# Kernel optimization log

Measured on AMD Instinct MI355X. Metric: run time of the kernel, lower is better.

The kernel has to match this reference:

```python
import jax, jax.numpy as jnp
import numpy as np
import math

V, D, H, L, T, B = 50257, 1024, 16, 8, 1024, 4
HD = D // H
EPS = 1e-5


def setup_inputs() -> dict:
    key = jax.random.key(0)
    ks = jax.random.split(key, 8)
    s = 0.02
    inp = {
        'context': jax.random.randint(ks[0], (B, T), 0, V, dtype=jnp.int32),
        'targets': jax.random.randint(ks[1], (B, T), 0, V, dtype=jnp.int32),
        'wte': jax.random.normal(ks[2], (V, D), jnp.float32) * s,  # tied with lm_head
        'wpe': jax.random.normal(ks[3], (T, D), jnp.float32) * s,
        'ln1_g': jnp.ones((L, D), jnp.float32), 'ln1_b': jnp.zeros((L, D), jnp.float32),
        'w_attn': jax.random.normal(ks[4], (L, 3 * D, D), jnp.float32) * s,
        'w_proj': jax.random.normal(ks[5], (L, D, D), jnp.float32) * s,
        'ln2_g': jnp.ones((L, D), jnp.float32), 'ln2_b': jnp.zeros((L, D), jnp.float32),
        'w_fc': jax.random.normal(ks[6], (L, 4 * D, D), jnp.float32) * s,
        'w_out': jax.random.normal(ks[7], (L, D, 4 * D), jnp.float32) * s,
        'lnf_g': jnp.ones((D,), jnp.float32), 'lnf_b': jnp.zeros((D,), jnp.float32),
    }
    return inp


def layer_norm(x, g, b):
    mu = jnp.mean(x, axis=-1, keepdims=True)
    var = jnp.var(x, axis=-1, keepdims=True)
    return (x - mu) * jax.lax.rsqrt(var + EPS) * g + b


def attention(x, w_attn, w_proj):
    # x: [B,T,D]; w_attn: [3D,D] (torch Linear convention: y = x @ W^T)
    qkv = x @ w_attn.T  # [B,T,3D]
    q, k, v = jnp.split(qkv, 3, axis=-1)
    q = q.reshape(B, T, H, HD).transpose(0, 2, 1, 3)  # [B,H,T,hd]
    k = k.reshape(B, T, H, HD).transpose(0, 2, 1, 3)
    v = v.reshape(B, T, H, HD).transpose(0, 2, 1, 3)
    att = jnp.einsum('bhtd,bhsd->bhts', q, k) * (1.0 / math.sqrt(HD))
    causal = jnp.tril(jnp.ones((T, T), dtype=bool))
    att = jnp.where(causal, att, -jnp.inf)
    att = jax.nn.softmax(att, axis=-1)
    y = jnp.einsum('bhts,bhsd->bhtd', att, v)
    y = y.transpose(0, 2, 1, 3).reshape(B, T, D)
    return y @ w_proj.T


def mlp(x, w_fc, w_out):
    h = jax.nn.gelu(x @ w_fc.T, approximate=False)  # exact GELU = torch nn.GELU()
    return h @ w_out.T


def reference(context, targets, wte, wpe, ln1_g, ln1_b, w_attn, w_proj,
              ln2_g, ln2_b, w_fc, w_out, lnf_g, lnf_b):
    x = wte[context] + wpe[jnp.arange(T)]  # [B,T,D]
    for i in range(L):
        x = x + attention(layer_norm(x, ln1_g[i], ln1_b[i]), w_attn[i], w_proj[i])
        x = x + mlp(layer_norm(x, ln2_g[i], ln2_b[i]), w_fc[i], w_out[i])
    x = layer_norm(x, lnf_g, lnf_b)
    logits = x @ wte.T  # tied lm_head, [B,T,V]
    # cross entropy with ignore_index=-1
    logp = jax.nn.log_softmax(logits, axis=-1)
    tgt = targets.reshape(-1)
    valid = tgt != -1
    safe_tgt = jnp.where(valid, tgt, 0)
    nll = -jnp.take_along_axis(logp.reshape(-1, V), safe_tgt[:, None], axis=-1)[:, 0]
    loss = jnp.sum(jnp.where(valid, nll, 0.0)) / jnp.maximum(jnp.sum(valid), 1)
    return logits, loss
```

## Files before the change

### kernel.cpp

```cpp
#include <hip/hip_runtime.h>
#include <cstdint>

#define V_SIZE 50257
#define V_PAD  50432
#define D_DIM  1024
#define H_NUM  16
#define L_NUM  8
#define T_LEN  1024
#define B_NUM  4
#define HD_DIM 64
#define M_ROWS 4096
#define LN_EPS 1e-5f

typedef __attribute__((ext_vector_type(8))) __bf16 bf16x8;
typedef __attribute__((ext_vector_type(4))) float f32x4;
typedef __attribute__((ext_vector_type(8))) unsigned short u16x8;

__device__ __forceinline__ unsigned short f2bf(float f) {
  unsigned u = __builtin_bit_cast(unsigned, f);
  u += 0x7fffu + ((u >> 16) & 1u);
  return (unsigned short)(u >> 16);
}

__device__ __forceinline__ void gload_lds16(const void* g, void* l) {
  typedef const __attribute__((address_space(1))) unsigned int* gp_t;
  typedef __attribute__((address_space(3))) unsigned int* lp_t;
  __builtin_amdgcn_global_load_lds((gp_t)g, (lp_t)l, 16, 0, 0);
}

__device__ __forceinline__ f32x4 mfma16(bf16x8 a, bf16x8 b, f32x4 c) {
  return __builtin_amdgcn_mfma_f32_16x16x32_bf16(a, b, c, 0, 0, 0);
}

#define BARSB() { __builtin_amdgcn_s_barrier(); __builtin_amdgcn_sched_barrier(0); }
#define SCHB()  __builtin_amdgcn_sched_barrier(0)

__global__ __launch_bounds__(256) void embed_kernel(const int* __restrict__ ctx,
                                                    const float* __restrict__ wte,
                                                    const float* __restrict__ wpe,
                                                    float* __restrict__ x) {
  int i = blockIdx.x * blockDim.x + threadIdx.x;
  if (i >= M_ROWS * D_DIM) return;
  int bt = i / D_DIM, d = i - bt * D_DIM;
  int t = bt & (T_LEN - 1);
  x[i] = wte[(size_t)ctx[bt] * D_DIM + d] + wpe[(size_t)t * D_DIM + d];
}

__global__ __launch_bounds__(256) void conv_layer_kernel(const float* __restrict__ wa,
                                                         const float* __restrict__ wp,
                                                         const float* __restrict__ wf,
                                                         const float* __restrict__ wo,
                                                         unsigned short* __restrict__ oa,
                                                         unsigned short* __restrict__ op,
                                                         unsigned short* __restrict__ of,
                                                         unsigned short* __restrict__ oo) {
  long i = (long)(blockIdx.x * 256 + threadIdx.x) * 8;
  const float* src; unsigned short* dst; long off;
  if (i < 3145728L)      { src = wa; dst = oa; off = i; }
  else if (i < 4194304L) { src = wp; dst = op; off = i - 3145728L; }
  else if (i < 8388608L) { src = wf; dst = of; off = i - 4194304L; }
  else                   { src = wo; dst = oo; off = i - 8388608L; }
  float4 v0 = *(const float4*)(src + off);
  float4 v1 = *(const float4*)(src + off + 4);
  u16x8 o;
  o[0] = f2bf(v0.x); o[1] = f2bf(v0.y); o[2] = f2bf(v0.z); o[3] = f2bf(v0.w);
  o[4] = f2bf(v1.x); o[5] = f2bf(v1.y); o[6] = f2bf(v1.z); o[7] = f2bf(v1.w);
  *(u16x8*)(dst + off) = o;
}

__global__ __launch_bounds__(256) void conv_kernel(const float* __restrict__ in,
                                                   unsigned short* __restrict__ out, long n) {
  long i = (long)(blockIdx.x * 256 + threadIdx.x) * 8;
  if (i >= n) return;
  float4 v0 = *(const float4*)(in + i);
  float4 v1 = *(const float4*)(in + i + 4);
  u16x8 o;
  o[0] = f2bf(v0.x); o[1] = f2bf(v0.y); o[2] = f2bf(v0.z); o[3] = f2bf(v0.w);
  o[4] = f2bf(v1.x); o[5] = f2bf(v1.y); o[6] = f2bf(v1.z); o[7] = f2bf(v1.w);
  *(u16x8*)(out + i) = o;
}

__global__ __launch_bounds__(256) void layernorm_kernel(const float* __restrict__ x,
                                                        const float* __restrict__ g,
                                                        const float* __restrict__ b,
                                                        unsigned short* __restrict__ o) {
  int r = blockIdx.x;
  int tid = threadIdx.x;
  const float* row = x + (size_t)r * D_DIM;
  float4 v = *(const float4*)(row + tid * 4);
  float s  = v.x + v.y + v.z + v.w;
  float s2 = v.x * v.x + v.y * v.y + v.z * v.z + v.w * v.w;
  #pragma unroll
  for (int off = 32; off; off >>= 1) {
    s  += __shfl_xor(s, off);
    s2 += __shfl_xor(s2, off);
  }
  __shared__ float a1[4], a2[4];
  int w = tid >> 6, lane = tid & 63;
  if (lane == 0) { a1[w] = s; a2[w] = s2; }
  __syncthreads();
  s  = a1[0] + a1[1] + a1[2] + a1[3];
  s2 = a2[0] + a2[1] + a2[2] + a2[3];
  float mu  = s * (1.0f / D_DIM);
  float var = s2 * (1.0f / D_DIM) - mu * mu;
  float rs  = rsqrtf(var + LN_EPS);
  int d = tid * 4;
  float4 gv = *(const float4*)(g + d);
  float4 bv = *(const float4*)(b + d);
  ushort4 ov;
  ov.x = f2bf((v.x - mu) * rs * gv.x + bv.x);
  ov.y = f2bf((v.y - mu) * rs * gv.y + bv.y);
  ov.z = f2bf((v.z - mu) * rs * gv.z + bv.z);
  ov.w = f2bf((v.w - mu) * rs * gv.w + bv.w);
  *(ushort4*)(o + (size_t)r * D_DIM + d) = ov;
}

template<int EPI>
__global__ __launch_bounds__(256) void mfma_gemm(const unsigned short* __restrict__ A,
                                                 const unsigned short* __restrict__ W,
                                                 const float* R, void* Cout,
                                                 int K, int ldc, int nreal) {
  __shared__ unsigned short As[128 * 32];
  __shared__ unsigned short Bs[128 * 32];
  const int tid  = threadIdx.x;
  const int wave = tid >> 6, lane = tid & 63;
  const int wr = wave >> 1, wc = wave & 1;
  const long row0 = (long)blockIdx.y * 128;
  const long col0 = (long)blockIdx.x * 128;
  f32x4 acc[4][4] = {};
  const int frow = lane & 15;
  const int fk   = (lane >> 4) * 8;
  const int b0 = wave * 2048 + lane * 16;
  for (int k0 = 0; k0 < K; k0 += 32) {
    #pragma unroll
    for (int c = 0; c < 2; ++c) {
      int b = b0 + c * 1024;
      int r = b >> 6, ke = (b & 63) >> 1;
      gload_lds16(A + (row0 + r) * (long)K + k0 + ke, (char*)As + b);
      gload_lds16(W + (col0 + r) * (long)K + k0 + ke, (char*)Bs + b);
    }
    __syncthreads();
    bf16x8 af[4], bfr[4];
    #pragma unroll
    for (int i = 0; i < 4; ++i)
      af[i] = *(const bf16x8*)(As + (wr * 64 + i * 16 + frow) * 32 + fk);
    #pragma unroll
    for (int j = 0; j < 4; ++j)
      bfr[j] = *(const bf16x8*)(Bs + (wc * 64 + j * 16 + frow) * 32 + fk);
    #pragma unroll
    for (int i = 0; i < 4; ++i)
      #pragma unroll
      for (int j = 0; j < 4; ++j)
        acc[i][j] = mfma16(af[i], bfr[j], acc[i][j]);
    __syncthreads();
  }
  const int crow = (lane >> 4) * 4;
  const int ccol = lane & 15;
  #pragma unroll
  for (int i = 0; i < 4; ++i) {
    #pragma unroll
    for (int r = 0; r < 4; ++r) {
      long row = row0 + wr * 64 + i * 16 + crow + r;
      #pragma unroll
      for (int j = 0; j < 4; ++j) {
        long col = col0 + wc * 64 + j * 16 + ccol;
        float v = acc[i][j][r];
        if (EPI == 1) {
          ((float*)Cout)[row * (long)ldc + col] = v + R[row * (long)ldc + col];
        } else {
          ((float*)Cout)[row * (long)ldc + col] = v;
        }
      }
    }
  }
}

__device__ __forceinline__ void stage_chunk8(const unsigned short* __restrict__ base,
                                             long rbase, int K, long gk,
                                             char* cb, int tid) {
  #pragma unroll
  for (int j = 0; j < 2; ++j) {
    int db = j * 8192 + tid * 16;
    int lb = db ^ (((db >> 7) & 3) << 4);
    long r = lb >> 6;
    int e = (lb & 63) >> 1;
    gload_lds16(base + (rbase + r) * (long)K + gk + e, cb + db);
  }
}

__device__ __forceinline__ bf16x8 rdfrag(const char* cb, int rr, int lhi) {
  int p = (rr << 6) + (lhi << 4);
  p ^= ((rr >> 1) & 3) << 4;
  return *(const bf16x8*)(cb + p);
}

template<int EPI>
__global__ __launch_bounds__(512, 1) void gemm8p(const unsigned short* __restrict__ A,
                                                 const unsigned short* __restrict__ W,
                                                 void* Cout, int K, int ldc, int nreal,
                                                 int nbx, int xcd) {
  __shared__ char lds[131072];
  const int tid  = threadIdx.x;
  const int lane = tid & 63;
  const int wave = tid >> 6;
  const int wr = wave >> 2, wc = wave & 3;
  const int lhi = lane >> 4, llo = lane & 15;
  int bid = blockIdx.x;
  if (xcd) { int per = (int)gridDim.x >> 3; bid = (bid & 7) * per + (bid >> 3); }
  const int brow = bid % nbx;
  const int bcol = bid / nbx;
  const long row0 = (long)brow * 256;
  const long col0 = (long)bcol * 256;
  char* Ab0 = (char*)lds;
  char* Bb0 = (char*)lds + 65536;
  const int nt = K >> 6;

  stage_chunk8(W, col0, K, 0,  Bb0,         tid);
  stage_chunk8(A, row0, K, 0,  Ab0,         tid);
  stage_chunk8(W, col0, K, 32, Bb0 + 16384, tid);
  stage_chunk8(A, row0, K, 32, Ab0 + 16384, tid);
  stage_chunk8(W, col0, K, 64, Bb0 + 32768, tid);
  stage_chunk8(A, row0, K, 64, Ab0 + 32768, tid);
  stage_chunk8(W, col0, K, 96, Bb0 + 49152, tid);
  asm volatile("s_waitcnt vmcnt(10)" ::: "memory");
  BARSB();

  const int arow  = wr * 128 + llo;
  const int brow_ = wc * 64 + llo;

  bf16x8 aa0[4], aa1[4], bb0[4], bb1[4];
  #pragma unroll
  for (int m = 0; m < 4; ++m) aa0[m] = rdfrag(Ab0, arow + m * 16, lhi);
  #pragma unroll
  for (int n = 0; n < 4; ++n) bb0[n] = rdfrag(Bb0, brow_ + n * 16, lhi);

  f32x4 acc[8][4] = {};
  for (int t = 0; t < nt; ++t) {
    char* Ac = Ab0 + (t & 1) * 32768;
    char* Bc = Bb0 + (t & 1) * 32768;
    char* An = Ab0 + ((t + 1) & 1) * 32768;
    char* Bn = Bb0 + ((t + 1) & 1) * 32768;
    #pragma unroll
    for (int m = 0; m < 4; ++m) aa1[m] = rdfrag(Ac, arow + 64 + m * 16, lhi);
    asm volatile("s_waitcnt lgkmcnt(4)" ::: "memory");
    SCHB();
    if (t + 1 < nt) stage_chunk8(A, row0, K, (long)(t + 1) * 64 + 32, An + 16384, tid);
    __builtin_amdgcn_s_setprio(1);
    #pragma unroll
    for (int m = 0; m < 4; ++m)
      #pragma unroll
      for (int n = 0; n < 4; ++n)
        acc[m][n] = mfma16(aa0[m], bb0[n], acc[m][n]);
    __builtin_amdgcn_s_setprio(0);
    SCHB();
    if (t < nt - 1) { asm volatile("s_waitcnt vmcnt(8)" ::: "memory"); }
    else            { asm volatile("s_waitcnt vmcnt(0)" ::: "memory"); }
    BARSB();
    #pragma unroll
    for (int m = 0; m < 4; ++m) aa0[m] = rdfrag(Ac + 16384, arow + m * 16, lhi);
    #pragma unroll
    for (int n = 0; n < 4; ++n) bb1[n] = rdfrag(Bc + 16384, brow_ + n * 16, lhi);
    asm volatile("s_waitcnt lgkmcnt(8)" ::: "memory");
    SCHB();
    if (t + 2 < nt) stage_chunk8(W, col0, K, (long)(t + 2) * 64, Bc, tid);
    __builtin_amdgcn_s_setprio(1);
    #pragma unroll
    for (int m = 0; m < 4; ++m)
      #pragma unroll
      for (int n = 0; n < 4; ++n)
        acc[m + 4][n] = mfma16(aa1[m], bb0[n], acc[m + 4][n]);
    __builtin_amdgcn_s_setprio(0);
    SCHB();
    BARSB();
    #pragma unroll
    for (int m = 0; m < 4; ++m) aa1[m] = rdfrag(Ac + 16384, arow + 64 + m * 16, lhi);
    asm volatile("s_waitcnt lgkmcnt(4)" ::: "memory");
    SCHB();
    if (t + 2 < nt) stage_chunk8(A, row0, K, (long)(t + 2) * 64, Ac, tid);
    __builtin_amdgcn_s_setprio(1);
    #pragma unroll
    for (int m = 0; m < 4; ++m)
      #pragma unroll
      for (int n = 0; n < 4; ++n)
        acc[m][n] = mfma16(aa0[m], bb1[n], acc[m][n]);
    __builtin_amdgcn_s_setprio(0);
    SCHB();
    if (t <= nt - 3)      { asm volatile("s_waitcnt vmcnt(8)" ::: "memory"); }
    else if (t == nt - 2) { asm volatile("s_waitcnt vmcnt(4)" ::: "memory"); }
    else                  { asm volatile("s_waitcnt vmcnt(0)" ::: "memory"); }
    BARSB();
    if (t + 1 < nt) {
      #pragma unroll
      for (int m = 0; m < 4; ++m) aa0[m] = rdfrag(An, arow + m * 16, lhi);
      #pragma unroll
      for (int n = 0; n < 4; ++n) bb0[n] = rdfrag(Bn, brow_ + n * 16, lhi);
      asm volatile("s_waitcnt lgkmcnt(8)" ::: "memory");
    } else {
      asm volatile("s_waitcnt lgkmcnt(0)" ::: "memory");
    }
    SCHB();
    if (t + 2 < nt) stage_chunk8(W, col0, K, (long)(t + 2) * 64 + 32, Bc + 16384, tid);
    __builtin_amdgcn_s_setprio(1);
    #pragma unroll
    for (int m = 0; m < 4; ++m)
      #pragma unroll
      for (int n = 0; n < 4; ++n)
        acc[m + 4][n] = mfma16(aa1[m], bb1[n], acc[m + 4][n]);
    __builtin_amdgcn_s_setprio(0);
    SCHB();
    BARSB();
  }

  #pragma unroll
  for (int mi = 0; mi < 8; ++mi) {
    #pragma unroll
    for (int rg = 0; rg < 4; ++rg) {
      long row = row0 + wr * 128 + mi * 16 + lhi * 4 + rg;
      #pragma unroll
      for (int n = 0; n < 4; ++n) {
        long col = col0 + wc * 64 + n * 16 + llo;
        float v = acc[mi][n][rg];
        if (EPI == 0) {
          if (col < nreal) ((float*)Cout)[row * (long)ldc + col] = v;
        } else if (EPI == 2) {
          float gl = 0.5f * v * (1.0f + erff(v * 0.70710678118654752440f));
          ((unsigned short*)Cout)[row * (long)ldc + col] = f2bf(gl);
        } else {
          ((unsigned short*)Cout)[row * (long)ldc + col] = f2bf(v);
        }
      }
    }
  }
}

__global__ __launch_bounds__(256) void flash_attn_kernel(const unsigned short* __restrict__ qkv,
                                                         unsigned short* __restrict__ y) {
  __shared__ unsigned short Kls[64 * 64];
  __shared__ unsigned short Vtls[64 * 64];
  __shared__ unsigned short Pls[4][16 * 64];
  const int tid = threadIdx.x, wave = tid >> 6, lane = tid & 63;
  const int qt = blockIdx.x;
  const int h = blockIdx.y & (H_NUM - 1), b = blockIdx.y >> 4;
  const int q0 = qt * 64;
  const int lhi = lane >> 4, llo = lane & 15;

  const int qrow = q0 + wave * 16 + llo;
  const unsigned short* qptr =
      qkv + ((size_t)(b * T_LEN + qrow)) * 3072 + h * HD_DIM + lhi * 8;
  const bf16x8 qa0 = *(const bf16x8*)qptr;
  const bf16x8 qa1 = *(const bf16x8*)(qptr + 32);

  f32x4 o[4] = {};
  float m[4] = {-1e30f, -1e30f, -1e30f, -1e30f};
  float l[4] = {0.f, 0.f, 0.f, 0.f};

  const unsigned short* kg = qkv + (size_t)b * T_LEN * 3072 + D_DIM + h * HD_DIM;
  const unsigned short* vg = kg + D_DIM;

  const int krow = tid >> 2, kcol = (tid & 3) * 16;
  const int vs0 = (tid >> 3) * 2, vd0 = (tid & 7) * 8;

  const int ntiles = qt + 1;
  for (int st = 0; st < ntiles; ++st) {
    const int s0 = st * 64;
    {
      const unsigned short* src = kg + (size_t)(s0 + krow) * 3072 + kcol;
      u16x8 a = *(const u16x8*)src;
      u16x8 c = *(const u16x8*)(src + 8);
      int base = krow * 128 + kcol * 2;
      int sw = (krow & 7) << 4;
      *(u16x8*)((char*)Kls + ((base) ^ sw))      = a;
      *(u16x8*)((char*)Kls + ((base + 16) ^ sw)) = c;
    }
    {
      const unsigned short* src = vg + (size_t)(s0 + vs0) * 3072 + vd0;
      u16x8 a = *(const u16x8*)src;
      u16x8 c = *(const u16x8*)(src + 3072);
      #pragma unroll
      for (int j = 0; j < 8; ++j) {
        int d = vd0 + j;
        unsigned val = (unsigned)a[j] | ((unsigned)c[j] << 16);
        *(unsigned*)((char*)Vtls + ((d * 128 + vs0 * 2) ^ ((d & 7) << 4))) = val;
      }
    }
    __syncthreads();

    f32x4 s_acc[4] = {};
    #pragma unroll
    for (int kt = 0; kt < 4; ++kt) {
      int kr = kt * 16 + llo;
      int sw = (kr & 7) << 4;
      bf16x8 kb0 = *(const bf16x8*)((char*)Kls + ((kr * 128 + lhi * 16) ^ sw));
      bf16x8 kb1 = *(const bf16x8*)((char*)Kls + ((kr * 128 + 64 + lhi * 16) ^ sw));
      s_acc[kt] = mfma16(qa0, kb0, s_acc[kt]);
      s_acc[kt] = mfma16(qa1, kb1, s_acc[kt]);
    }

    float p[4][4];
    float tmax[4] = {-1e30f, -1e30f, -1e30f, -1e30f};
    const int qg = q0 + wave * 16 + lhi * 4;
    #pragma unroll
    for (int kt = 0; kt < 4; ++kt) {
      int ks = s0 + kt * 16 + llo;
      #pragma unroll
      for (int r = 0; r < 4; ++r) {
        float sv = (ks <= qg + r) ? s_acc[kt][r] * 0.125f : -1e30f;
        p[kt][r] = sv;
        tmax[r] = fmaxf(tmax[r], sv);
      }
    }
    #pragma unroll
    for (int r = 0; r < 4; ++r) {
      #pragma unroll
      for (int off = 1; off < 16; off <<= 1)
        tmax[r] = fmaxf(tmax[r], __shfl_xor(tmax[r], off));
      float mn = fmaxf(m[r], tmax[r]);
      float corr = __expf(m[r] - mn);
      m[r] = mn;
      float ps = 0.f;
      #pragma unroll
      for (int kt = 0; kt < 4; ++kt) {
        p[kt][r] = __expf(p[kt][r] - mn);
        ps += p[kt][r];
      }
      #pragma unroll
      for (int off = 1; off < 16; off <<= 1)
        ps += __shfl_xor(ps, off);
      l[r] = l[r] * corr + ps;
      #pragma unroll
      for (int dt = 0; dt < 4; ++dt) o[dt][r] *= corr;
    }

    unsigned short* pw = Pls[wave];
    #pragma unroll
    for (int r = 0; r < 4; ++r) {
      int q = lhi * 4 + r;
      int sw = (q & 7) << 4;
      #pragma unroll
      for (int kt = 0; kt < 4; ++kt) {
        int k = kt * 16 + llo;
        *(unsigned short*)((char*)pw + ((q * 128 + k * 2) ^ sw)) = f2bf(p[kt][r]);
      }
    }
    asm volatile("s_waitcnt lgkmcnt(0)" ::: "memory");

    int psw = (llo & 7) << 4;
    bf16x8 pa0 = *(const bf16x8*)((char*)pw + ((llo * 128 + lhi * 16) ^ psw));
    bf16x8 pa1 = *(const bf16x8*)((char*)pw + ((llo * 128 + 64 + lhi * 16) ^ psw));
    #pragma unroll
    for (int dt = 0; dt < 4; ++dt) {
      int vr = dt * 16 + llo;
      int sw = (vr & 7) << 4;
      bf16x8 vb0 = *(const bf16x8*)((char*)Vtls + ((vr * 128 + lhi * 16) ^ sw));
      bf16x8 vb1 = *(const bf16x8*)((char*)Vtls + ((vr * 128 + 64 + lhi * 16) ^ sw));
      o[dt] = mfma16(pa0, vb0, o[dt]);
      o[dt] = mfma16(pa1, vb1, o[dt]);
    }
    __syncthreads();
  }

  #pragma unroll
  for (int r = 0; r < 4; ++r) {
    long row = q0 + wave * 16 + lhi * 4 + r;
    float inv = 1.0f / l[r];
    #pragma unroll
    for (int dt = 0; dt < 4; ++dt) {
      long col = h * HD_DIM + dt * 16 + llo;
      y[(row + (size_t)b * T_LEN) * D_DIM + col] = f2bf(o[dt][r] * inv);
    }
  }
}

__global__ __launch_bounds__(256) void loss_rows_kernel(const float* __restrict__ logits,
                                                        const int* __restrict__ tgt,
                                                        float* __restrict__ nll,
                                                        float* __restrict__ vld) {
  int r = blockIdx.x;
  int tid = threadIdx.x;
  const float* row = logits + (size_t)r * V_SIZE;
  float lm = -1e30f, ls = 0.f;
  for (int i = tid; i < V_SIZE; i += 256) {
    float v = row[i];
    float nm = fmaxf(lm, v);
    ls = ls * __expf(lm - nm) + __expf(v - nm);
    lm = nm;
  }
  #pragma unroll
  for (int off = 1; off < 64; off <<= 1) {
    float om = __shfl_xor(lm, off);
    float os = __shfl_xor(ls, off);
    float nm = fmaxf(lm, om);
    ls = ls * __expf(lm - nm) + os * __expf(om - nm);
    lm = nm;
  }
  __shared__ float sm[4], ss[4];
  int w = tid >> 6, lane = tid & 63;
  if (lane == 0) { sm[w] = lm; ss[w] = ls; }
  __syncthreads();
  if (tid == 0) {
    lm = sm[0]; ls = ss[0];
    #pragma unroll
    for (int i = 1; i < 4; ++i) {
      float nm = fmaxf(lm, sm[i]);
      ls = ls * __expf(lm - nm) + ss[i] * __expf(sm[i] - nm);
      lm = nm;
    }
    int tg = tgt[r];
    if (tg != -1) { nll[r] = lm + logf(ls) - row[tg]; vld[r] = 1.0f; }
    else          { nll[r] = 0.f;                     vld[r] = 0.f; }
  }
}

__global__ __launch_bounds__(256) void loss_reduce_kernel(const float* __restrict__ nll,
                                                          const float* __restrict__ vld,
                                                          float* __restrict__ out) {
  int tid = threadIdx.x;
  float s = 0.f, c = 0.f;
  for (int i = tid; i < M_ROWS; i += 256) { s += nll[i]; c += vld[i]; }
  #pragma unroll
  for (int off = 32; off; off >>= 1) { s += __shfl_xor(s, off); c += __shfl_xor(c, off); }
  __shared__ float s1[4], s2[4];
  int w = tid >> 6, lane = tid & 63;
  if (lane == 0) { s1[w] = s; s2[w] = c; }
  __syncthreads();
  if (tid == 0) {
    s = s1[0] + s1[1] + s1[2] + s1[3];
    c = s2[0] + s2[1] + s2[2] + s2[3];
    out[0] = s / fmaxf(c, 1.0f);
  }
}

extern "C" void kernel_launch(void* const* d_in, const int* in_sizes, int n_in,
                              void* d_out, int out_size, void* d_ws, size_t ws_size,
                              hipStream_t stream) {
  const int*   ctx    = (const int*)d_in[0];
  const int*   tgt    = (const int*)d_in[1];
  const float* wte    = (const float*)d_in[2];
  const float* wpe    = (const float*)d_in[3];
  const float* ln1_g  = (const float*)d_in[4];
  const float* ln1_b  = (const float*)d_in[5];
  const float* w_attn = (const float*)d_in[6];
  const float* w_proj = (const float*)d_in[7];
  const float* ln2_g  = (const float*)d_in[8];
  const float* ln2_b  = (const float*)d_in[9];
  const float* w_fc   = (const float*)d_in[10];
  const float* w_out  = (const float*)d_in[11];
  const float* lnf_g  = (const float*)d_in[12];
  const float* lnf_b  = (const float*)d_in[13];

  float* outp   = (float*)d_out;
  float* logits = outp;
  float* loss   = outp + (size_t)M_ROWS * V_SIZE;

  char* ws = (char*)d_ws;
  float*          x      = (float*)(ws + 0);
  unsigned short* xn     = (unsigned short*)(ws + 16777216);
  unsigned short* qkv    = (unsigned short*)(ws + 25165824);
  unsigned short* y      = (unsigned short*)(ws + 50331648);
  unsigned short* h      = (unsigned short*)(ws + 58720256);
  unsigned short* wa_bf  = (unsigned short*)(ws + 92274688);
  unsigned short* wp_bf  = (unsigned short*)(ws + 98566144);
  unsigned short* wf_bf  = (unsigned short*)(ws + 100663296);
  unsigned short* wo_bf  = (unsigned short*)(ws + 109051904);
  unsigned short* wte_bf = (unsigned short*)(ws + 25165824);
  float*          nll    = (float*)(ws + 128450560);
  float*          vld    = (float*)(ws + 128466944);

  embed_kernel<<<(M_ROWS * D_DIM + 255) / 256, 256, 0, stream>>>(ctx, wte, wpe, x);

  for (int l = 0; l < L_NUM; ++l) {
    conv_layer_kernel<<<6144, 256, 0, stream>>>(
        w_attn + (size_t)l * 3 * D_DIM * D_DIM, w_proj + (size_t)l * D_DIM * D_DIM,
        w_fc + (size_t)l * 4 * D_DIM * D_DIM, w_out + (size_t)l * D_DIM * 4 * D_DIM,
        wa_bf, wp_bf, wf_bf, wo_bf);
    layernorm_kernel<<<M_ROWS, 256, 0, stream>>>(x, ln1_g + l * D_DIM, ln1_b + l * D_DIM, xn);
    gemm8p<3><<<12 * 16, 512, 0, stream>>>(
        xn, wa_bf, qkv, D_DIM, 3 * D_DIM, 3 * D_DIM, 16, 1);
    flash_attn_kernel<<<dim3(T_LEN / 64, B_NUM * H_NUM), 256, 0, stream>>>(qkv, y);
    mfma_gemm<1><<<dim3(D_DIM / 128, M_ROWS / 128), 256, 0, stream>>>(
        y, wp_bf, x, x, D_DIM, D_DIM, D_DIM);
    layernorm_kernel<<<M_ROWS, 256, 0, stream>>>(x, ln2_g + l * D_DIM, ln2_b + l * D_DIM, xn);
    gemm8p<2><<<16 * 16, 512, 0, stream>>>(
        xn, wf_bf, h, D_DIM, 4 * D_DIM, 4 * D_DIM, 16, 1);
    mfma_gemm<1><<<dim3(D_DIM / 128, M_ROWS / 128), 256, 0, stream>>>(
        h, wo_bf, x, x, 4 * D_DIM, D_DIM, D_DIM);
  }

  layernorm_kernel<<<M_ROWS, 256, 0, stream>>>(x, lnf_g, lnf_b, xn);
  conv_kernel<<<25129, 256, 0, stream>>>(wte, wte_bf, (long)V_SIZE * D_DIM);
  hipMemsetAsync(wte_bf + (size_t)V_SIZE * D_DIM, 0,
                 (size_t)(V_PAD - V_SIZE) * D_DIM * sizeof(unsigned short), stream);
  gemm8p<0><<<197 * 16, 512, 0, stream>>>(
      xn, wte_bf, logits, D_DIM, V_SIZE, V_SIZE, 16, 1);
  loss_rows_kernel<<<M_ROWS, 256, 0, stream>>>(logits, tgt, nll, vld);
  loss_reduce_kernel<<<1, 256, 0, stream>>>(nll, vld, loss);
}
```

Measured before the change: 3.443 ms.

## Fuse partial log-softmax stats into logits GEMM epilogue; widen attention query tile

The lm_head GEMM epilogue now computes per-row partial max and sum-of-exp for each column block and writes them to workspace. A small combine kernel merges the partials and gathers the target logit, so the full logits matrix no longer has to be re-read. Flash attention now processes 128 query rows per block with 512 threads, and K and V staging are split across the two thread halves. This adds epilogue ALU/shuffle work, a block sync in the GEMM, and coarser causal load balance in attention.

```diff
diff --git a/kernel.cpp b/kernel.cpp
--- a/kernel.cpp
+++ b/kernel.cpp
@@ -3,6 +3,7 @@
 
 #define V_SIZE 50257
 #define V_PAD  50432
+#define NCB    197
 #define D_DIM  1024
 #define H_NUM  16
 #define L_NUM  8
@@ -198,7 +199,9 @@
 __global__ __launch_bounds__(512, 1) void gemm8p(const unsigned short* __restrict__ A,
                                                  const unsigned short* __restrict__ W,
                                                  void* Cout, int K, int ldc, int nreal,
-                                                 int nbx, int xcd) {
+                                                 int nbx, int xcd,
+                                                 float* __restrict__ pmax,
+                                                 float* __restrict__ psum) {
   __shared__ char lds[131072];
   const int tid  = threadIdx.x;
   const int lane = tid & 63;
@@ -331,17 +334,65 @@
       }
     }
   }
-}
-
-__global__ __launch_bounds__(256) void flash_attn_kernel(const unsigned short* __restrict__ qkv,
+
+  if (EPI == 0) {
+    float* red = (float*)lds;
+    #pragma unroll
+    for (int mi = 0; mi < 8; ++mi) {
+      #pragma unroll
+      for (int rg = 0; rg < 4; ++rg) {
+        float mx = -1e30f;
+        #pragma unroll
+        for (int n = 0; n < 4; ++n) {
+          long col = col0 + wc * 64 + n * 16 + llo;
+          if (col < nreal) mx = fmaxf(mx, acc[mi][n][rg]);
+        }
+        float se = 0.f;
+        #pragma unroll
+        for (int n = 0; n < 4; ++n) {
+          long col = col0 + wc * 64 + n * 16 + llo;
+          if (col < nreal) se += __expf(acc[mi][n][rg] - mx);
+        }
+        #pragma unroll
+        for (int off = 1; off < 16; off <<= 1) {
+          float om = __shfl_xor(mx, off);
+          float os = __shfl_xor(se, off);
+          float M = fmaxf(mx, om);
+          se = se * __expf(mx - M) + os * __expf(om - M);
+          mx = M;
+        }
+        if (llo == 0) {
+          int rloc = wr * 128 + mi * 16 + lhi * 4 + rg;
+          red[(rloc * 4 + wc) * 2 + 0] = mx;
+          red[(rloc * 4 + wc) * 2 + 1] = se;
+        }
+      }
+    }
+    __syncthreads();
+    if (tid < 256) {
+      float m = red[(tid * 4 + 0) * 2 + 0], s = red[(tid * 4 + 0) * 2 + 1];
+      #pragma unroll
+      for (int wci = 1; wci < 4; ++wci) {
+        float om = red[(tid * 4 + wci) * 2 + 0], os = red[(tid * 4 + wci) * 2 + 1];
+        float M = fmaxf(m, om);
+        s = s * __expf(m - M) + os * __expf(om - M);
+        m = M;
+      }
+      pmax[(long)bcol * M_ROWS + row0 + tid] = m;
+      psum[(long)bcol * M_ROWS + row0 + tid] = s;
+    }
+  }
+}
+
+__global__ __launch_bounds__(512) void flash_attn_kernel(const unsigned short* __restrict__ qkv,
                                                          unsigned short* __restrict__ y) {
   __shared__ unsigned short Kls[64 * 64];
   __shared__ unsigned short Vtls[64 * 64];
-  __shared__ unsigned short Pls[4][16 * 64];
+  __shared__ unsigned short Pls[8][16 * 64];
   const int tid = threadIdx.x, wave = tid >> 6, lane = tid & 63;
   const int qt = blockIdx.x;
   const int h = blockIdx.y & (H_NUM - 1), b = blockIdx.y >> 4;
-  const int q0 = qt * 64;
+  const int q0 = qt * 128;
   const int lhi = lane >> 4, llo = lane & 15;
 
   const int qrow = q0 + wave * 16 + llo;
@@ -357,13 +408,24 @@
   const unsigned short* kg = qkv + (size_t)b * T_LEN * 3072 + D_DIM + h * HD_DIM;
   const unsigned short* vg = kg + D_DIM;
 
-  const int krow = tid >> 2, kcol = (tid & 3) * 16;
-  const int vs0 = (tid >> 3) * 2, vd0 = (tid & 7) * 8;
-
-  const int ntiles = qt + 1;
+  const int vs0 = ((tid & 255) >> 3) * 2, vd0 = (tid & 7) * 8;
+  const int t2 = tid - 256;
+  const int krow = (t2 & 255) >> 2, kcol = (t2 & 3) * 16;
+
+  const int ntiles = 2 * qt + 2;
   for (int st = 0; st < ntiles; ++st) {
     const int s0 = st * 64;
-    {
+    if (tid < 256) {
+      const unsigned short* src = vg + (size_t)(s0 + vs0) * 3072 + vd0;
+      u16x8 a = *(const u16x8*)src;
+      u16x8 c = *(const u16x8*)(src + 3072);
+      #pragma unroll
+      for (int j = 0; j < 8; ++j) {
+        int d = vd0 + j;
+        unsigned val = (unsigned)a[j] | ((unsigned)c[j] << 16);
+        *(unsigned*)((char*)Vtls + ((d * 128 + vs0 * 2) ^ ((d & 7) << 4))) = val;
+      }
+    } else {
       const unsigned short* src = kg + (size_t)(s0 + krow) * 3072 + kcol;
       u16x8 a = *(const u16x8*)src;
       u16x8 c = *(const u16x8*)(src + 8);
@@ -372,17 +434,6 @@
       *(u16x8*)((char*)Kls + ((base) ^ sw))      = a;
       *(u16x8*)((char*)Kls + ((base + 16) ^ sw)) = c;
     }
-    {
-      const unsigned short* src = vg + (size_t)(s0 + vs0) * 3072 + vd0;
-      u16x8 a = *(const u16x8*)src;
-      u16x8 c = *(const u16x8*)(src + 3072);
-      #pragma unroll
-      for (int j = 0; j < 8; ++j) {
-        int d = vd0 + j;
-        unsigned val = (unsigned)a[j] | ((unsigned)c[j] << 16);
-        *(unsigned*)((char*)Vtls + ((d * 128 + vs0 * 2) ^ ((d & 7) << 4))) = val;
-      }
-    }
     __syncthreads();
 
     f32x4 s_acc[4] = {};
@@ -471,44 +522,24 @@
   }
 }
 
-__global__ __launch_bounds__(256) void loss_rows_kernel(const float* __restrict__ logits,
-                                                        const int* __restrict__ tgt,
-                                                        float* __restrict__ nll,
-                                                        float* __restrict__ vld) {
-  int r = blockIdx.x;
-  int tid = threadIdx.x;
-  const float* row = logits + (size_t)r * V_SIZE;
-  float lm = -1e30f, ls = 0.f;
-  for (int i = tid; i < V_SIZE; i += 256) {
-    float v = row[i];
-    float nm = fmaxf(lm, v);
-    ls = ls * __expf(lm - nm) + __expf(v - nm);
-    lm = nm;
-  }
-  #pragma unroll
-  for (int off = 1; off < 64; off <<= 1) {
-    float om = __shfl_xor(lm, off);
-    float os = __shfl_xor(ls, off);
-    float nm = fmaxf(lm, om);
-    ls = ls * __expf(lm - nm) + os * __expf(om - nm);
-    lm = nm;
-  }
-  __shared__ float sm[4], ss[4];
-  int w = tid >> 6, lane = tid & 63;
-  if (lane == 0) { sm[w] = lm; ss[w] = ls; }
-  __syncthreads();
-  if (tid == 0) {
-    lm = sm[0]; ls = ss[0];
-    #pragma unroll
-    for (int i = 1; i < 4; ++i) {
-      float nm = fmaxf(lm, sm[i]);
-      ls = ls * __expf(lm - nm) + ss[i] * __expf(sm[i] - nm);
-      lm = nm;
-    }
-    int tg = tgt[r];
-    if (tg != -1) { nll[r] = lm + logf(ls) - row[tg]; vld[r] = 1.0f; }
-    else          { nll[r] = 0.f;                     vld[r] = 0.f; }
-  }
+__global__ __launch_bounds__(256) void loss_combine_kernel(const float* __restrict__ pmax,
+                                                           const float* __restrict__ psum,
+                                                           const float* __restrict__ logits,
+                                                           const int* __restrict__ tgt,
+                                                           float* __restrict__ nll,
+                                                           float* __restrict__ vld) {
+  int r = blockIdx.x * 256 + threadIdx.x;
+  float m = pmax[r], s = psum[r];
+  for (int cb = 1; cb < NCB; ++cb) {
+    float om = pmax[(long)cb * M_ROWS + r];
+    float os = psum[(long)cb * M_ROWS + r];
+    float M = fmaxf(m, om);
+    s = s * __expf(m - M) + os * __expf(om - M);
+    m = M;
+  }
+  int tg = tgt[r];
+  if (tg != -1) { nll[r] = m + logf(s) - logits[(size_t)r * V_SIZE + tg]; vld[r] = 1.0f; }
+  else          { nll[r] = 0.f;                                           vld[r] = 0.f; }
 }
 
 __global__ __launch_bounds__(256) void loss_reduce_kernel(const float* __restrict__ nll,
@@ -565,6 +596,8 @@
   unsigned short* wte_bf = (unsigned short*)(ws + 25165824);
   float*          nll    = (float*)(ws + 128450560);
   float*          vld    = (float*)(ws + 128466944);
+  float*          pmax   = (float*)(ws + 128483328);
+  float*          psum   = (float*)(ws + 131710976);
 
   embed_kernel<<<(M_ROWS * D_DIM + 255) / 256, 256, 0, stream>>>(ctx, wte, wpe, x);
 
@@ -575,13 +608,13 @@
         wa_bf, wp_bf, wf_bf, wo_bf);
     layernorm_kernel<<<M_ROWS, 256, 0, stream>>>(x, ln1_g + l * D_DIM, ln1_b + l * D_DIM, xn);
     gemm8p<3><<<12 * 16, 512, 0, stream>>>(
-        xn, wa_bf, qkv, D_DIM, 3 * D_DIM, 3 * D_DIM, 16, 1);
-    flash_attn_kernel<<<dim3(T_LEN / 64, B_NUM * H_NUM), 256, 0, stream>>>(qkv, y);
+        xn, wa_bf, qkv, D_DIM, 3 * D_DIM, 3 * D_DIM, 16, 1, nullptr, nullptr);
+    flash_attn_kernel<<<dim3(T_LEN / 128, B_NUM * H_NUM), 512, 0, stream>>>(qkv, y);
     mfma_gemm<1><<<dim3(D_DIM / 128, M_ROWS / 128), 256, 0, stream>>>(
         y, wp_bf, x, x, D_DIM, D_DIM, D_DIM);
     layernorm_kernel<<<M_ROWS, 256, 0, stream>>>(x, ln2_g + l * D_DIM, ln2_b + l * D_DIM, xn);
     gemm8p<2><<<16 * 16, 512, 0, stream>>>(
-        xn, wf_bf, h, D_DIM, 4 * D_DIM, 4 * D_DIM, 16, 1);
+        xn, wf_bf, h, D_DIM, 4 * D_DIM, 4 * D_DIM, 16, 1, nullptr, nullptr);
     mfma_gemm<1><<<dim3(D_DIM / 128, M_ROWS / 128), 256, 0, stream>>>(
         h, wo_bf, x, x, 4 * D_DIM, D_DIM, D_DIM);
   }
@@ -590,8 +623,8 @@
   conv_kernel<<<25129, 256, 0, stream>>>(wte, wte_bf, (long)V_SIZE * D_DIM);
   hipMemsetAsync(wte_bf + (size_t)V_SIZE * D_DIM, 0,
                  (size_t)(V_PAD - V_SIZE) * D_DIM * sizeof(unsigned short), stream);
-  gemm8p<0><<<197 * 16, 512, 0, stream>>>(
-      xn, wte_bf, logits, D_DIM, V_SIZE, V_SIZE, 16, 1);
-  loss_rows_kernel<<<M_ROWS, 256, 0, stream>>>(logits, tgt, nll, vld);
+  gemm8p<0><<<NCB * 16, 512, 0, stream>>>(
+      xn, wte_bf, logits, D_DIM, V_SIZE, V_SIZE, 16, 1, pmax, psum);
+  loss_combine_kernel<<<M_ROWS / 256, 256, 0, stream>>>(pmax, psum, logits, tgt, nll, vld);
   loss_reduce_kernel<<<1, 256, 0, stream>>>(nll, vld, loss);
 }
```

New measurement: 3.245 ms. 5.8% less time.
